# Optimization experiments

Hardware: AMD Instinct MI355X
Metric: run time of the kernel (lower is better)

## Reference

```python
import jax, jax.numpy as jnp
import numpy as np

NUM_CLUSTERS = 64
DIM = 512
ALPHA = 100.0
EPS = 1e-12  # torch F.normalize eps


def setup_inputs() -> dict:
    key = jax.random.key(0)
    k1, k2 = jax.random.split(key)
    x1 = jax.random.normal(k1, (30, DIM, 28, 28), dtype=jnp.float32)
    centroids = jax.random.uniform(k2, (NUM_CLUSTERS, DIM), dtype=jnp.float32)
    # _init_params: conv weight = 2*alpha*centroids (1x1 conv), bias = -alpha*||centroid||
    conv_w = 2.0 * ALPHA * centroids
    conv_b = -ALPHA * jnp.linalg.norm(centroids, axis=1)
    return {"x1": x1, "centroids": centroids, "conv_w": conv_w, "conv_b": conv_b}


def _l2norm(v, axis):
    n = jnp.sqrt(jnp.sum(v * v, axis=axis, keepdims=True))
    return v / jnp.maximum(n, EPS)


def reference(x1, centroids, conv_w, conv_b):
    T, C, H, W = x1.shape
    K, D = centroids.shape
    x = x1.reshape(T, C, H * W)            # [T, C, N]
    x = _l2norm(x, axis=1)                 # normalize_input: L2 over channel dim
    # 1x1 conv == matmul over channels: logits [T, K, N]
    logits = jnp.einsum('kc,tcn->tkn', conv_w, x) + conv_b[None, :, None]
    a = jax.nn.softmax(logits, axis=1)     # soft assignment over clusters
    # vlad[t,k,c] = sum_n a[t,k,n]*(x[t,c,n] - centroids[k,c])
    # rewritten as two small matmuls, avoiding the [K,C,N] residual tensor
    vlad = jnp.einsum('tkn,tcn->tkc', a, x) - a.sum(axis=-1)[:, :, None] * centroids[None]
    vlad = _l2norm(vlad, axis=2)           # intra-normalization over feature dim
    v = vlad.reshape(T, K * D)
    v = _l2norm(v, axis=1)                 # global L2 normalization
    return v.sum(axis=0, keepdims=True)    # [1, K*D] accumulated over 30 timesteps
```

## Files before the change

kernel.cpp:

```cpp
#include <hip/hip_runtime.h>
#include <math.h>

#define T_ 30
#define C_ 512
#define N_ 784
#define NA_ 800
#define XPITCH 520
#define EPSV 1e-12f

typedef __attribute__((ext_vector_type(8))) short bf16x8;
typedef __attribute__((ext_vector_type(4))) float f32x4;

__device__ __forceinline__ unsigned short f2bf(float f) {
    union { float f; unsigned int u; } v; v.f = f;
    unsigned int r = (v.u + 0x7FFFu + ((v.u >> 16) & 1u)) >> 16;
    return (unsigned short)r;
}
__device__ __forceinline__ float bf2f(unsigned short h) {
    union { unsigned int u; float f; } v; v.u = ((unsigned int)h) << 16;
    return v.f;
}

__global__ void k_prep(const float* __restrict__ w, unsigned short* __restrict__ wh,
                       unsigned short* __restrict__ wl) {
    int idx = blockIdx.x * 256 + threadIdx.x;
    float v = w[idx];
    unsigned short h = f2bf(v);
    wh[idx] = h;
    wl[idx] = f2bf(v - bf2f(h));
}

__global__ __launch_bounds__(256) void k_assign(
    const float* __restrict__ x, const unsigned short* __restrict__ wh,
    const unsigned short* __restrict__ wl, const float* __restrict__ b,
    unsigned short* __restrict__ aT, float* __restrict__ asum)
{
    __shared__ __align__(16) char smem[2 * 16 * XPITCH * 2];
    unsigned short* xh = (unsigned short*)smem;
    unsigned short* xl = xh + 16 * XPITCH;
    float* red = (float*)smem;
    __shared__ float ssq[4][16];
    __shared__ float invl[16];

    int t = blockIdx.y, n0 = blockIdx.x * 16;
    int tid = threadIdx.x;
    int w = tid >> 6, L = tid & 63, lid = L & 15, quad = L >> 4;

    int nseg = (tid & 3) * 4;
    int crow = tid >> 2;
    float ss0 = 0.f, ss1 = 0.f, ss2 = 0.f, ss3 = 0.f;
    #pragma unroll
    for (int p = 0; p < 8; ++p) {
        int c = p * 64 + crow;
        float4 q = *reinterpret_cast<const float4*>(
            x + ((size_t)t * C_ + c) * N_ + n0 + nseg);
        ss0 = fmaf(q.x, q.x, ss0); ss1 = fmaf(q.y, q.y, ss1);
        ss2 = fmaf(q.z, q.z, ss2); ss3 = fmaf(q.w, q.w, ss3);
        float vv[4] = {q.x, q.y, q.z, q.w};
        #pragma unroll
        for (int j = 0; j < 4; ++j) {
            unsigned short h = f2bf(vv[j]);
            xh[(nseg + j) * XPITCH + c] = h;
            xl[(nseg + j) * XPITCH + c] = f2bf(vv[j] - bf2f(h));
        }
    }
    #pragma unroll
    for (int m = 4; m <= 32; m <<= 1) {
        ss0 += __shfl_xor(ss0, m, 64); ss1 += __shfl_xor(ss1, m, 64);
        ss2 += __shfl_xor(ss2, m, 64); ss3 += __shfl_xor(ss3, m, 64);
    }
    if (L < 4) {
        ssq[w][L * 4 + 0] = ss0; ssq[w][L * 4 + 1] = ss1;
        ssq[w][L * 4 + 2] = ss2; ssq[w][L * 4 + 3] = ss3;
    }
    __syncthreads();
    if (tid < 16) {
        float s = ssq[0][tid] + ssq[1][tid] + ssq[2][tid] + ssq[3][tid];
        invl[tid] = 1.0f / fmaxf(sqrtf(s), EPSV);
    }

    f32x4 acc[4];
    #pragma unroll
    for (int mt = 0; mt < 4; ++mt)
        #pragma unroll
        for (int r = 0; r < 4; ++r) acc[mt][r] = 0.f;

    #pragma unroll
    for (int ks = 0; ks < 4; ++ks) {
        int cs = w * 128 + ks * 32;
        bf16x8 bh = *reinterpret_cast<const bf16x8*>(&xh[lid * XPITCH + cs + quad * 8]);
        bf16x8 bl = *reinterpret_cast<const bf16x8*>(&xl[lid * XPITCH + cs + quad * 8]);
        #pragma unroll
        for (int mt = 0; mt < 4; ++mt) {
            bf16x8 ah = *reinterpret_cast<const bf16x8*>(wh + (size_t)(mt * 16 + lid) * C_ + cs + quad * 8);
            bf16x8 al = *reinterpret_cast<const bf16x8*>(wl + (size_t)(mt * 16 + lid) * C_ + cs + quad * 8);
            acc[mt] = __builtin_amdgcn_mfma_f32_16x16x32_bf16(ah, bh, acc[mt], 0, 0, 0);
            acc[mt] = __builtin_amdgcn_mfma_f32_16x16x32_bf16(al, bh, acc[mt], 0, 0, 0);
            acc[mt] = __builtin_amdgcn_mfma_f32_16x16x32_bf16(ah, bl, acc[mt], 0, 0, 0);
        }
    }
    __syncthreads();
    {
        float* rp = red + w * (16 * 68);
        #pragma unroll
        for (int mt = 0; mt < 4; ++mt)
            *reinterpret_cast<f32x4*>(&rp[lid * 68 + mt * 16 + quad * 4]) = acc[mt];
    }
    __syncthreads();

    float bk = b[L];
    float asl = 0.f;
    unsigned short av[4];
    #pragma unroll
    for (int i = 0; i < 4; ++i) {
        int n = w * 4 + i;
        float v = red[0 * 1088 + n * 68 + L] + red[1 * 1088 + n * 68 + L]
                + red[2 * 1088 + n * 68 + L] + red[3 * 1088 + n * 68 + L];
        float inv = invl[n];
        v = fmaf(v, inv, bk);
        float mx = v;
        #pragma unroll
        for (int m = 1; m <= 32; m <<= 1) mx = fmaxf(mx, __shfl_xor(mx, m, 64));
        float e = __expf(v - mx);
        float se = e;
        #pragma unroll
        for (int m = 1; m <= 32; m <<= 1) se += __shfl_xor(se, m, 64);
        float a = e / se;
        av[i] = f2bf(a * inv);
        asl += a;
    }
    atomicAdd(&asum[t * 64 + L], asl);
    ushort4 st; st.x = av[0]; st.y = av[1]; st.z = av[2]; st.w = av[3];
    *reinterpret_cast<ushort4*>(aT + ((size_t)t * 64 + L) * NA_ + n0 + w * 4) = st;
}

__global__ __launch_bounds__(256) void k_vlad(
    const float* __restrict__ x, const unsigned short* __restrict__ aT,
    const float* __restrict__ asum, const float* __restrict__ cent,
    float* __restrict__ vlad, float* __restrict__ g2)
{
    __shared__ float red[4][16 * 68];
    int t = blockIdx.y, c0 = blockIdx.x * 16;
    int tid = threadIdx.x;
    int w = tid >> 6, L = tid & 63, lid = L & 15, quad = L >> 4;

    f32x4 acc[4];
    #pragma unroll
    for (int mt = 0; mt < 4; ++mt)
        #pragma unroll
        for (int r = 0; r < 4; ++r) acc[mt][r] = 0.f;

    const float* xrow = x + ((size_t)t * C_ + c0 + lid) * N_;
    const unsigned short* ab = aT + (size_t)t * 64 * NA_;

    for (int s = w; s < 25; s += 4) {
        int nb = s * 32 + quad * 8;
        int nbc = nb > 776 ? 776 : nb;
        float4 x0 = *reinterpret_cast<const float4*>(xrow + nbc);
        float4 x1 = *reinterpret_cast<const float4*>(xrow + nbc + 4);
        bf16x8 bb;
        bb[0] = (short)f2bf(x0.x); bb[1] = (short)f2bf(x0.y);
        bb[2] = (short)f2bf(x0.z); bb[3] = (short)f2bf(x0.w);
        bb[4] = (short)f2bf(x1.x); bb[5] = (short)f2bf(x1.y);
        bb[6] = (short)f2bf(x1.z); bb[7] = (short)f2bf(x1.w);
        #pragma unroll
        for (int mt = 0; mt < 4; ++mt) {
            bf16x8 af = *reinterpret_cast<const bf16x8*>(ab + (size_t)(mt * 16 + lid) * NA_ + nb);
            acc[mt] = __builtin_amdgcn_mfma_f32_16x16x32_bf16(af, bb, acc[mt], 0, 0, 0);
        }
    }
    {
        float* rp = &red[w][0];
        #pragma unroll
        for (int mt = 0; mt < 4; ++mt)
            *reinterpret_cast<f32x4*>(&rp[lid * 68 + mt * 16 + quad * 4]) = acc[mt];
    }
    __syncthreads();

    int k = tid >> 2, cs4 = (tid & 3) * 4;
    float as = asum[t * 64 + k];
    float4 cv = *reinterpret_cast<const float4*>(cent + k * C_ + c0 + cs4);
    float4 vout;
    float s2 = 0.f;
    #pragma unroll
    for (int j = 0; j < 4; ++j) {
        int cc = cs4 + j;
        float v = red[0][cc * 68 + k] + red[1][cc * 68 + k]
                + red[2][cc * 68 + k] + red[3][cc * 68 + k];
        v -= as * ((const float*)&cv)[j];
        ((float*)&vout)[j] = v;
        s2 = fmaf(v, v, s2);
    }
    *reinterpret_cast<float4*>(vlad + ((size_t)t * 64 + k) * C_ + c0 + cs4) = vout;
    s2 += __shfl_xor(s2, 1, 64);
    s2 += __shfl_xor(s2, 2, 64);
    if ((tid & 3) == 0) atomicAdd(&g2[t * 64 + k], s2);
}

__global__ __launch_bounds__(256) void k_out(
    const float* __restrict__ vlad, const float* __restrict__ g2,
    float* __restrict__ out)
{
    __shared__ float intr[1920];
    __shared__ float gl[1920];
    __shared__ float sinv[T_];
    int tid = threadIdx.x;
    for (int i = tid; i < 1920; i += 256) {
        float s = g2[i];
        gl[i] = s;
        intr[i] = 1.0f / fmaxf(sqrtf(s), EPSV);
    }
    __syncthreads();
    if (tid < T_) {
        float s = 0.f;
        #pragma unroll 8
        for (int k = 0; k < 64; ++k) {
            float iv = intr[tid * 64 + k];
            s += gl[tid * 64 + k] * iv * iv;
        }
        sinv[tid] = 1.0f / fmaxf(sqrtf(s), EPSV);
    }
    __syncthreads();
    int idx = blockIdx.x * 256 + tid;
    int k = idx >> 9;
    float s = 0.f;
    #pragma unroll 5
    for (int t = 0; t < T_; ++t)
        s += vlad[(size_t)t * 32768 + idx] * intr[t * 64 + k] * sinv[t];
    out[idx] = s;
}

extern "C" void kernel_launch(void* const* d_in, const int* in_sizes, int n_in,
                              void* d_out, int out_size, void* d_ws, size_t ws_size,
                              hipStream_t stream) {
    const float* x    = (const float*)d_in[0];
    const float* cent = (const float*)d_in[1];
    const float* w    = (const float*)d_in[2];
    const float* b    = (const float*)d_in[3];
    float* out = (float*)d_out;

    char* p = (char*)d_ws;
    unsigned short* wh = (unsigned short*)p;  p += 65536;
    unsigned short* wl = (unsigned short*)p;  p += 65536;
    float* asum = (float*)p;                  p += 1920 * 4;
    float* g2   = (float*)p;                  p += 1920 * 4;
    unsigned short* aT = (unsigned short*)p;  p += (size_t)T_ * 64 * NA_ * 2;
    float* vlad = (float*)p;                  p += (size_t)T_ * 64 * C_ * 4;

    k_prep<<<128, 256, 0, stream>>>(w, wh, wl);
    hipMemsetAsync(asum, 0, 2 * 1920 * 4, stream);
    hipMemsetAsync(aT, 0, (size_t)T_ * 64 * NA_ * 2, stream);
    k_assign<<<dim3(49, T_), 256, 0, stream>>>(x, wh, wl, b, aT, asum);
    k_vlad<<<dim3(32, T_), 256, 0, stream>>>(x, aT, asum, cent, vlad, g2);
    k_out<<<128, 256, 0, stream>>>(vlad, g2, out);
}
```

Before: 150.9 us.

## Add transpose pre-pass producing bf16 split layouts and column sum-of-squares

Adds a new kernel that reads x once, transposes it through shared memory into channel-contiguous bf16 hi/lo arrays for the assignment GEMM, writes a bf16 N-major copy for the VLAD GEMM, and accumulates per-pixel sum of squares with atomics. k_assign then loads operands straight from global memory instead of doing a strided fp32 gather and an in-LDS transpose. k_vlad reads pre-converted bf16 instead of converting fp32 on the fly. The cost is an extra launch plus writing and re-reading about three bf16 copies of x, which is more total memory traffic.

```diff
diff --git a/kernel.cpp b/kernel.cpp
--- a/kernel.cpp
+++ b/kernel.cpp
@@ -4,8 +4,8 @@
 #define T_ 30
 #define C_ 512
 #define N_ 784
+#define NP_ 832
 #define NA_ 800
-#define XPITCH 520
 #define EPSV 1e-12f
 
 typedef __attribute__((ext_vector_type(8))) short bf16x8;
@@ -30,54 +30,86 @@
     wl[idx] = f2bf(v - bf2f(h));
 }
 
+__global__ __launch_bounds__(256) void k_trans(
+    const float* __restrict__ x, unsigned short* __restrict__ xh,
+    unsigned short* __restrict__ xl, unsigned short* __restrict__ xbn,
+    float* __restrict__ sumsq)
+{
+    __shared__ float sx[64][65];
+    __shared__ float wred[4][64];
+    int n0 = blockIdx.x * 64, c0 = blockIdx.y * 64, t = blockIdx.z;
+    int tid = threadIdx.x;
+    int cr = tid >> 4, li = tid & 15;
+    int w = tid >> 6;
+    float ss[4] = {0.f, 0.f, 0.f, 0.f};
+
+    #pragma unroll
+    for (int j = 0; j < 4; ++j) {
+        int cl = j * 16 + cr;
+        int n = n0 + li * 4;
+        float4 q = make_float4(0.f, 0.f, 0.f, 0.f);
+        if (n < N_)
+            q = *reinterpret_cast<const float4*>(x + ((size_t)t * C_ + c0 + cl) * N_ + n);
+        ss[0] = fmaf(q.x, q.x, ss[0]); ss[1] = fmaf(q.y, q.y, ss[1]);
+        ss[2] = fmaf(q.z, q.z, ss[2]); ss[3] = fmaf(q.w, q.w, ss[3]);
+        sx[cl][li * 4 + 0] = q.x; sx[cl][li * 4 + 1] = q.y;
+        sx[cl][li * 4 + 2] = q.z; sx[cl][li * 4 + 3] = q.w;
+    }
+    #pragma unroll
+    for (int i = 0; i < 4; ++i) {
+        ss[i] += __shfl_xor(ss[i], 16, 64);
+        ss[i] += __shfl_xor(ss[i], 32, 64);
+    }
+    if (((tid >> 4) & 3) == 0) {
+        wred[w][li * 4 + 0] = ss[0]; wred[w][li * 4 + 1] = ss[1];
+        wred[w][li * 4 + 2] = ss[2]; wred[w][li * 4 + 3] = ss[3];
+    }
+    __syncthreads();
+    if (tid < 64 && n0 + tid < N_) {
+        float s = wred[0][tid] + wred[1][tid] + wred[2][tid] + wred[3][tid];
+        atomicAdd(&sumsq[t * N_ + n0 + tid], s);
+    }
+    {
+        int li2 = tid & 15, nr = tid >> 4;
+        #pragma unroll
+        for (int j = 0; j < 4; ++j) {
+            int nl = nr + j * 16;
+            float v0 = sx[li2 * 4 + 0][nl], v1 = sx[li2 * 4 + 1][nl];
+            float v2 = sx[li2 * 4 + 2][nl], v3 = sx[li2 * 4 + 3][nl];
+            ushort4 h, l;
+            h.x = f2bf(v0); l.x = f2bf(v0 - bf2f(h.x));
+            h.y = f2bf(v1); l.y = f2bf(v1 - bf2f(h.y));
+            h.z = f2bf(v2); l.z = f2bf(v2 - bf2f(h.z));
+            h.w = f2bf(v3); l.w = f2bf(v3 - bf2f(h.w));
+            size_t o = ((size_t)t * NP_ + n0 + nl) * C_ + c0 + li2 * 4;
+            *reinterpret_cast<ushort4*>(xh + o) = h;
+            *reinterpret_cast<ushort4*>(xl + o) = l;
+        }
+    }
+    #pragma unroll
+    for (int j = 0; j < 4; ++j) {
+        int cl = j * 16 + cr;
+        int n = n0 + li * 4;
+        if (n < NA_) {
+            ushort4 h;
+            h.x = f2bf(sx[cl][li * 4 + 0]); h.y = f2bf(sx[cl][li * 4 + 1]);
+            h.z = f2bf(sx[cl][li * 4 + 2]); h.w = f2bf(sx[cl][li * 4 + 3]);
+            *reinterpret_cast<ushort4*>(xbn + ((size_t)t * C_ + c0 + cl) * NA_ + n) = h;
+        }
+    }
+}
+
 __global__ __launch_bounds__(256) void k_assign(
-    const float* __restrict__ x, const unsigned short* __restrict__ wh,
-    const unsigned short* __restrict__ wl, const float* __restrict__ b,
+    const unsigned short* __restrict__ xh, const unsigned short* __restrict__ xl,
+    const unsigned short* __restrict__ wh, const unsigned short* __restrict__ wl,
+    const float* __restrict__ b, const float* __restrict__ sumsq,
     unsigned short* __restrict__ aT, float* __restrict__ asum)
 {
-    __shared__ __align__(16) char smem[2 * 16 * XPITCH * 2];
-    unsigned short* xh = (unsigned short*)smem;
-    unsigned short* xl = xh + 16 * XPITCH;
-    float* red = (float*)smem;
-    __shared__ float ssq[4][16];
-    __shared__ float invl[16];
-
+    __shared__ float red[4 * 16 * 68];
     int t = blockIdx.y, n0 = blockIdx.x * 16;
     int tid = threadIdx.x;
     int w = tid >> 6, L = tid & 63, lid = L & 15, quad = L >> 4;
-
-    int nseg = (tid & 3) * 4;
-    int crow = tid >> 2;
-    float ss0 = 0.f, ss1 = 0.f, ss2 = 0.f, ss3 = 0.f;
-    #pragma unroll
-    for (int p = 0; p < 8; ++p) {
-        int c = p * 64 + crow;
-        float4 q = *reinterpret_cast<const float4*>(
-            x + ((size_t)t * C_ + c) * N_ + n0 + nseg);
-        ss0 = fmaf(q.x, q.x, ss0); ss1 = fmaf(q.y, q.y, ss1);
-        ss2 = fmaf(q.z, q.z, ss2); ss3 = fmaf(q.w, q.w, ss3);
-        float vv[4] = {q.x, q.y, q.z, q.w};
-        #pragma unroll
-        for (int j = 0; j < 4; ++j) {
-            unsigned short h = f2bf(vv[j]);
-            xh[(nseg + j) * XPITCH + c] = h;
-            xl[(nseg + j) * XPITCH + c] = f2bf(vv[j] - bf2f(h));
-        }
-    }
-    #pragma unroll
-    for (int m = 4; m <= 32; m <<= 1) {
-        ss0 += __shfl_xor(ss0, m, 64); ss1 += __shfl_xor(ss1, m, 64);
-        ss2 += __shfl_xor(ss2, m, 64); ss3 += __shfl_xor(ss3, m, 64);
-    }
-    if (L < 4) {
-        ssq[w][L * 4 + 0] = ss0; ssq[w][L * 4 + 1] = ss1;
-        ssq[w][L * 4 + 2] = ss2; ssq[w][L * 4 + 3] = ss3;
-    }
-    __syncthreads();
-    if (tid < 16) {
-        float s = ssq[0][tid] + ssq[1][tid] + ssq[2][tid] + ssq[3][tid];
-        invl[tid] = 1.0f / fmaxf(sqrtf(s), EPSV);
-    }
+    int n_lane = n0 + lid;
 
     f32x4 acc[4];
     #pragma unroll
@@ -85,23 +117,25 @@
         #pragma unroll
         for (int r = 0; r < 4; ++r) acc[mt][r] = 0.f;
 
+    const unsigned short* bp  = xh + ((size_t)t * NP_ + n_lane) * C_ + w * 128 + quad * 8;
+    const unsigned short* blp = xl + ((size_t)t * NP_ + n_lane) * C_ + w * 128 + quad * 8;
+
     #pragma unroll
     for (int ks = 0; ks < 4; ++ks) {
-        int cs = w * 128 + ks * 32;
-        bf16x8 bh = *reinterpret_cast<const bf16x8*>(&xh[lid * XPITCH + cs + quad * 8]);
-        bf16x8 bl = *reinterpret_cast<const bf16x8*>(&xl[lid * XPITCH + cs + quad * 8]);
+        bf16x8 bh = *reinterpret_cast<const bf16x8*>(bp + ks * 32);
+        bf16x8 bl = *reinterpret_cast<const bf16x8*>(blp + ks * 32);
+        int cs = w * 128 + ks * 32 + quad * 8;
         #pragma unroll
         for (int mt = 0; mt < 4; ++mt) {
-            bf16x8 ah = *reinterpret_cast<const bf16x8*>(wh + (size_t)(mt * 16 + lid) * C_ + cs + quad * 8);
-            bf16x8 al = *reinterpret_cast<const bf16x8*>(wl + (size_t)(mt * 16 + lid) * C_ + cs + quad * 8);
+            bf16x8 ah = *reinterpret_cast<const bf16x8*>(wh + (size_t)(mt * 16 + lid) * C_ + cs);
+            bf16x8 al = *reinterpret_cast<const bf16x8*>(wl + (size_t)(mt * 16 + lid) * C_ + cs);
             acc[mt] = __builtin_amdgcn_mfma_f32_16x16x32_bf16(ah, bh, acc[mt], 0, 0, 0);
             acc[mt] = __builtin_amdgcn_mfma_f32_16x16x32_bf16(al, bh, acc[mt], 0, 0, 0);
             acc[mt] = __builtin_amdgcn_mfma_f32_16x16x32_bf16(ah, bl, acc[mt], 0, 0, 0);
         }
     }
-    __syncthreads();
     {
-        float* rp = red + w * (16 * 68);
+        float* rp = red + w * 1088;
         #pragma unroll
         for (int mt = 0; mt < 4; ++mt)
             *reinterpret_cast<f32x4*>(&rp[lid * 68 + mt * 16 + quad * 4]) = acc[mt];
@@ -116,7 +150,8 @@
         int n = w * 4 + i;
         float v = red[0 * 1088 + n * 68 + L] + red[1 * 1088 + n * 68 + L]
                 + red[2 * 1088 + n * 68 + L] + red[3 * 1088 + n * 68 + L];
-        float inv = invl[n];
+        float s = sumsq[t * N_ + n0 + n];
+        float inv = 1.0f / fmaxf(sqrtf(s), EPSV);
         v = fmaf(v, inv, bk);
         float mx = v;
         #pragma unroll
@@ -135,7 +170,7 @@
 }
 
 __global__ __launch_bounds__(256) void k_vlad(
-    const float* __restrict__ x, const unsigned short* __restrict__ aT,
+    const unsigned short* __restrict__ xbn, const unsigned short* __restrict__ aT,
     const float* __restrict__ asum, const float* __restrict__ cent,
     float* __restrict__ vlad, float* __restrict__ g2)
 {
@@ -150,19 +185,13 @@
         #pragma unroll
         for (int r = 0; r < 4; ++r) acc[mt][r] = 0.f;
 
-    const float* xrow = x + ((size_t)t * C_ + c0 + lid) * N_;
-    const unsigned short* ab = aT + (size_t)t * 64 * NA_;
-
+    const unsigned short* xr = xbn + ((size_t)t * C_ + c0 + lid) * NA_ + quad * 8;
+    const unsigned short* ab = aT + (size_t)t * 64 * NA_ + quad * 8;
+
+    #pragma unroll 2
     for (int s = w; s < 25; s += 4) {
-        int nb = s * 32 + quad * 8;
-        int nbc = nb > 776 ? 776 : nb;
-        float4 x0 = *reinterpret_cast<const float4*>(xrow + nbc);
-        float4 x1 = *reinterpret_cast<const float4*>(xrow + nbc + 4);
-        bf16x8 bb;
-        bb[0] = (short)f2bf(x0.x); bb[1] = (short)f2bf(x0.y);
-        bb[2] = (short)f2bf(x0.z); bb[3] = (short)f2bf(x0.w);
-        bb[4] = (short)f2bf(x1.x); bb[5] = (short)f2bf(x1.y);
-        bb[6] = (short)f2bf(x1.z); bb[7] = (short)f2bf(x1.w);
+        int nb = s * 32;
+        bf16x8 bb = *reinterpret_cast<const bf16x8*>(xr + nb);
         #pragma unroll
         for (int mt = 0; mt < 4; ++mt) {
             bf16x8 af = *reinterpret_cast<const bf16x8*>(ab + (size_t)(mt * 16 + lid) * NA_ + nb);
@@ -242,15 +271,20 @@
     char* p = (char*)d_ws;
     unsigned short* wh = (unsigned short*)p;  p += 65536;
     unsigned short* wl = (unsigned short*)p;  p += 65536;
-    float* asum = (float*)p;                  p += 1920 * 4;
-    float* g2   = (float*)p;                  p += 1920 * 4;
-    unsigned short* aT = (unsigned short*)p;  p += (size_t)T_ * 64 * NA_ * 2;
+    float* sumsq = (float*)p;                 p += 30 * 784 * 4;
+    float* asum  = (float*)p;                 p += 1920 * 4;
+    float* g2    = (float*)p;                 p += 1920 * 4;
+    unsigned short* aT  = (unsigned short*)p; p += (size_t)T_ * 64 * NA_ * 2;
+    unsigned short* xh  = (unsigned short*)p; p += (size_t)T_ * NP_ * C_ * 2;
+    unsigned short* xl  = (unsigned short*)p; p += (size_t)T_ * NP_ * C_ * 2;
+    unsigned short* xbn = (unsigned short*)p; p += (size_t)T_ * C_ * NA_ * 2;
     float* vlad = (float*)p;                  p += (size_t)T_ * 64 * C_ * 4;
 
     k_prep<<<128, 256, 0, stream>>>(w, wh, wl);
-    hipMemsetAsync(asum, 0, 2 * 1920 * 4, stream);
+    hipMemsetAsync(sumsq, 0, (30 * 784 + 2 * 1920) * 4, stream);
     hipMemsetAsync(aT, 0, (size_t)T_ * 64 * NA_ * 2, stream);
-    k_assign<<<dim3(49, T_), 256, 0, stream>>>(x, wh, wl, b, aT, asum);
-    k_vlad<<<dim3(32, T_), 256, 0, stream>>>(x, aT, asum, cent, vlad, g2);
+    k_trans<<<dim3(13, 8, T_), 256, 0, stream>>>(x, xh, xl, xbn, sumsq);
+    k_assign<<<dim3(49, T_), 256, 0, stream>>>(xh, xl, wh, wl, b, sumsq, aT, asum);
+    k_vlad<<<dim3(32, T_), 256, 0, stream>>>(xbn, aT, asum, cent, vlad, g2);
     k_out<<<128, 256, 0, stream>>>(vlad, g2, out);
 }
```

After: 163.1 us. +8.1%, slower.

## Retile assignment kernel to 64 positions per block with per-wave full reduction

Applied to the files above, without the earlier changes.

k_assign now handles 64 spatial positions per block instead of 16. Each wave owns 16 positions and accumulates the full channel reduction over four staged LDS chunks. The hi/lo bf16 split of x is packed into one 32-bit LDS word, and softmax runs directly from the MFMA accumulators. This removes the cross-wave LDS reduction and cuts redundant weight reloads per block. Padded positions are written as zeros, so the separate aT memset is dropped, and k_out loses one shared array. The cost is fewer blocks (390), which lowers parallelism, plus narrower scattered aT stores.

```diff
diff --git a/kernel.cpp b/kernel.cpp
--- a/kernel.cpp
+++ b/kernel.cpp
@@ -4,12 +4,13 @@
 #define T_ 30
 #define C_ 512
 #define N_ 784
-#define NA_ 800
-#define XPITCH 520
+#define NA_ 832
+#define PITCH 129
 #define EPSV 1e-12f
 
 typedef __attribute__((ext_vector_type(8))) short bf16x8;
 typedef __attribute__((ext_vector_type(4))) float f32x4;
+typedef __attribute__((ext_vector_type(4))) int i32x4;
 
 __device__ __forceinline__ unsigned short f2bf(float f) {
     union { float f; unsigned int u; } v; v.f = f;
@@ -35,49 +36,16 @@
     const unsigned short* __restrict__ wl, const float* __restrict__ b,
     unsigned short* __restrict__ aT, float* __restrict__ asum)
 {
-    __shared__ __align__(16) char smem[2 * 16 * XPITCH * 2];
-    unsigned short* xh = (unsigned short*)smem;
-    unsigned short* xl = xh + 16 * XPITCH;
-    float* red = (float*)smem;
-    __shared__ float ssq[4][16];
-    __shared__ float invl[16];
-
-    int t = blockIdx.y, n0 = blockIdx.x * 16;
+    __shared__ unsigned int xpk[64 * PITCH];
+    __shared__ float ssq[64];
+    int t = blockIdx.y, n0 = blockIdx.x * 64;
     int tid = threadIdx.x;
     int w = tid >> 6, L = tid & 63, lid = L & 15, quad = L >> 4;
-
-    int nseg = (tid & 3) * 4;
-    int crow = tid >> 2;
-    float ss0 = 0.f, ss1 = 0.f, ss2 = 0.f, ss3 = 0.f;
-    #pragma unroll
-    for (int p = 0; p < 8; ++p) {
-        int c = p * 64 + crow;
-        float4 q = *reinterpret_cast<const float4*>(
-            x + ((size_t)t * C_ + c) * N_ + n0 + nseg);
-        ss0 = fmaf(q.x, q.x, ss0); ss1 = fmaf(q.y, q.y, ss1);
-        ss2 = fmaf(q.z, q.z, ss2); ss3 = fmaf(q.w, q.w, ss3);
-        float vv[4] = {q.x, q.y, q.z, q.w};
-        #pragma unroll
-        for (int j = 0; j < 4; ++j) {
-            unsigned short h = f2bf(vv[j]);
-            xh[(nseg + j) * XPITCH + c] = h;
-            xl[(nseg + j) * XPITCH + c] = f2bf(vv[j] - bf2f(h));
-        }
-    }
-    #pragma unroll
-    for (int m = 4; m <= 32; m <<= 1) {
-        ss0 += __shfl_xor(ss0, m, 64); ss1 += __shfl_xor(ss1, m, 64);
-        ss2 += __shfl_xor(ss2, m, 64); ss3 += __shfl_xor(ss3, m, 64);
-    }
-    if (L < 4) {
-        ssq[w][L * 4 + 0] = ss0; ssq[w][L * 4 + 1] = ss1;
-        ssq[w][L * 4 + 2] = ss2; ssq[w][L * 4 + 3] = ss3;
-    }
-    __syncthreads();
-    if (tid < 16) {
-        float s = ssq[0][tid] + ssq[1][tid] + ssq[2][tid] + ssq[3][tid];
-        invl[tid] = 1.0f / fmaxf(sqrtf(s), EPSV);
-    }
+    int nseg = (tid & 15) * 4;
+    int crow = tid >> 4;
+
+    if (tid < 64) ssq[tid] = 0.f;
+    float ss[4] = {0.f, 0.f, 0.f, 0.f};
 
     f32x4 acc[4];
     #pragma unroll
@@ -85,53 +53,104 @@
         #pragma unroll
         for (int r = 0; r < 4; ++r) acc[mt][r] = 0.f;
 
-    #pragma unroll
-    for (int ks = 0; ks < 4; ++ks) {
-        int cs = w * 128 + ks * 32;
-        bf16x8 bh = *reinterpret_cast<const bf16x8*>(&xh[lid * XPITCH + cs + quad * 8]);
-        bf16x8 bl = *reinterpret_cast<const bf16x8*>(&xl[lid * XPITCH + cs + quad * 8]);
-        #pragma unroll
-        for (int mt = 0; mt < 4; ++mt) {
-            bf16x8 ah = *reinterpret_cast<const bf16x8*>(wh + (size_t)(mt * 16 + lid) * C_ + cs + quad * 8);
-            bf16x8 al = *reinterpret_cast<const bf16x8*>(wl + (size_t)(mt * 16 + lid) * C_ + cs + quad * 8);
-            acc[mt] = __builtin_amdgcn_mfma_f32_16x16x32_bf16(ah, bh, acc[mt], 0, 0, 0);
-            acc[mt] = __builtin_amdgcn_mfma_f32_16x16x32_bf16(al, bh, acc[mt], 0, 0, 0);
-            acc[mt] = __builtin_amdgcn_mfma_f32_16x16x32_bf16(ah, bl, acc[mt], 0, 0, 0);
-        }
-    }
-    __syncthreads();
-    {
-        float* rp = red + w * (16 * 68);
-        #pragma unroll
-        for (int mt = 0; mt < 4; ++mt)
-            *reinterpret_cast<f32x4*>(&rp[lid * 68 + mt * 16 + quad * 4]) = acc[mt];
-    }
-    __syncthreads();
-
-    float bk = b[L];
-    float asl = 0.f;
-    unsigned short av[4];
-    #pragma unroll
-    for (int i = 0; i < 4; ++i) {
-        int n = w * 4 + i;
-        float v = red[0 * 1088 + n * 68 + L] + red[1 * 1088 + n * 68 + L]
-                + red[2 * 1088 + n * 68 + L] + red[3 * 1088 + n * 68 + L];
-        float inv = invl[n];
-        v = fmaf(v, inv, bk);
-        float mx = v;
-        #pragma unroll
-        for (int m = 1; m <= 32; m <<= 1) mx = fmaxf(mx, __shfl_xor(mx, m, 64));
-        float e = __expf(v - mx);
-        float se = e;
-        #pragma unroll
-        for (int m = 1; m <= 32; m <<= 1) se += __shfl_xor(se, m, 64);
-        float a = e / se;
-        av[i] = f2bf(a * inv);
-        asl += a;
-    }
-    atomicAdd(&asum[t * 64 + L], asl);
-    ushort4 st; st.x = av[0]; st.y = av[1]; st.z = av[2]; st.w = av[3];
-    *reinterpret_cast<ushort4*>(aT + ((size_t)t * 64 + L) * NA_ + n0 + w * 4) = st;
+    for (int cc = 0; cc < 4; ++cc) {
+        #pragma unroll
+        for (int p = 0; p < 8; ++p) {
+            int cl = p * 16 + crow;
+            int c = cc * 128 + cl;
+            int n = n0 + nseg;
+            float4 q = make_float4(0.f, 0.f, 0.f, 0.f);
+            if (n < N_)
+                q = *reinterpret_cast<const float4*>(x + ((size_t)t * C_ + c) * N_ + n);
+            float vv[4] = {q.x, q.y, q.z, q.w};
+            #pragma unroll
+            for (int j = 0; j < 4; ++j) {
+                float v = vv[j];
+                ss[j] = fmaf(v, v, ss[j]);
+                union { float f; unsigned int u; } cv; cv.f = v;
+                unsigned int hiw = cv.u & 0xFFFF0000u;
+                union { unsigned int u; float f; } hv; hv.u = hiw;
+                unsigned int lo = f2bf(v - hv.f);
+                xpk[(nseg + j) * PITCH + cl] = hiw | lo;
+            }
+        }
+        if (cc == 3) {
+            #pragma unroll
+            for (int j = 0; j < 4; ++j) {
+                ss[j] += __shfl_xor(ss[j], 16, 64);
+                ss[j] += __shfl_xor(ss[j], 32, 64);
+            }
+            if ((tid & 48) == 0) {
+                #pragma unroll
+                for (int j = 0; j < 4; ++j) atomicAdd(&ssq[nseg + j], ss[j]);
+            }
+        }
+        __syncthreads();
+        #pragma unroll
+        for (int ks = 0; ks < 4; ++ks) {
+            int cl0 = ks * 32 + quad * 8;
+            unsigned int u[8];
+            #pragma unroll
+            for (int e = 0; e < 8; ++e)
+                u[e] = xpk[(w * 16 + lid) * PITCH + cl0 + e];
+            union { i32x4 v; bf16x8 b; } bh, bl;
+            #pragma unroll
+            for (int e2 = 0; e2 < 4; ++e2) {
+                bh.v[e2] = (int)((u[2 * e2] >> 16) | (u[2 * e2 + 1] & 0xFFFF0000u));
+                bl.v[e2] = (int)((u[2 * e2] & 0xFFFFu) | (u[2 * e2 + 1] << 16));
+            }
+            int cs = cc * 128 + ks * 32 + quad * 8;
+            #pragma unroll
+            for (int mt = 0; mt < 4; ++mt) {
+                bf16x8 ah = *reinterpret_cast<const bf16x8*>(wh + (size_t)(mt * 16 + lid) * C_ + cs);
+                bf16x8 al = *reinterpret_cast<const bf16x8*>(wl + (size_t)(mt * 16 + lid) * C_ + cs);
+                acc[mt] = __builtin_amdgcn_mfma_f32_16x16x32_bf16(ah, bh.b, acc[mt], 0, 0, 0);
+                acc[mt] = __builtin_amdgcn_mfma_f32_16x16x32_bf16(al, bh.b, acc[mt], 0, 0, 0);
+                acc[mt] = __builtin_amdgcn_mfma_f32_16x16x32_bf16(ah, bl.b, acc[mt], 0, 0, 0);
+            }
+        }
+        __syncthreads();
+    }
+
+    int n_lane = n0 + w * 16 + lid;
+    bool valid = n_lane < N_;
+    float inv = 0.f;
+    if (valid) inv = 1.0f / fmaxf(sqrtf(ssq[w * 16 + lid]), EPSV);
+
+    float lg[16];
+    float mx = -1e30f;
+    #pragma unroll
+    for (int mt = 0; mt < 4; ++mt) {
+        f32x4 bv = *reinterpret_cast<const f32x4*>(b + mt * 16 + quad * 4);
+        #pragma unroll
+        for (int r = 0; r < 4; ++r) {
+            float v = fmaf(acc[mt][r], inv, bv[r]);
+            lg[mt * 4 + r] = v;
+            mx = fmaxf(mx, v);
+        }
+    }
+    mx = fmaxf(mx, __shfl_xor(mx, 16, 64));
+    mx = fmaxf(mx, __shfl_xor(mx, 32, 64));
+    float se = 0.f;
+    #pragma unroll
+    for (int u = 0; u < 16; ++u) { lg[u] = __expf(lg[u] - mx); se += lg[u]; }
+    se += __shfl_xor(se, 16, 64);
+    se += __shfl_xor(se, 32, 64);
+    float rs = 1.0f / se;
+
+    size_t abase = (size_t)t * 64 * NA_ + n_lane;
+    #pragma unroll
+    for (int mt = 0; mt < 4; ++mt)
+        #pragma unroll
+        for (int r = 0; r < 4; ++r) {
+            int k = mt * 16 + quad * 4 + r;
+            float a = lg[mt * 4 + r] * rs;
+            aT[abase + (size_t)k * NA_] = valid ? f2bf(a * inv) : (unsigned short)0;
+            float ak = valid ? a : 0.f;
+            ak += __shfl_xor(ak, 1, 64); ak += __shfl_xor(ak, 2, 64);
+            ak += __shfl_xor(ak, 4, 64); ak += __shfl_xor(ak, 8, 64);
+            if (lid == 0) atomicAdd(&asum[t * 64 + k], ak);
+        }
 }
 
 __global__ __launch_bounds__(256) void k_vlad(
@@ -153,7 +172,7 @@
     const float* xrow = x + ((size_t)t * C_ + c0 + lid) * N_;
     const unsigned short* ab = aT + (size_t)t * 64 * NA_;
 
-    for (int s = w; s < 25; s += 4) {
+    for (int s = w; s < 26; s += 4) {
         int nb = s * 32 + quad * 8;
         int nbc = nb > 776 ? 776 : nb;
         float4 x0 = *reinterpret_cast<const float4*>(xrow + nbc);
@@ -202,21 +221,17 @@
     float* __restrict__ out)
 {
     __shared__ float intr[1920];
-    __shared__ float gl[1920];
     __shared__ float sinv[T_];
     int tid = threadIdx.x;
-    for (int i = tid; i < 1920; i += 256) {
-        float s = g2[i];
-        gl[i] = s;
-        intr[i] = 1.0f / fmaxf(sqrtf(s), EPSV);
-    }
+    for (int i = tid; i < 1920; i += 256)
+        intr[i] = 1.0f / fmaxf(sqrtf(g2[i]), EPSV);
     __syncthreads();
     if (tid < T_) {
         float s = 0.f;
         #pragma unroll 8
         for (int k = 0; k < 64; ++k) {
             float iv = intr[tid * 64 + k];
-            s += gl[tid * 64 + k] * iv * iv;
+            s += g2[tid * 64 + k] * iv * iv;
         }
         sinv[tid] = 1.0f / fmaxf(sqrtf(s), EPSV);
     }
@@ -249,8 +264,7 @@
 
     k_prep<<<128, 256, 0, stream>>>(w, wh, wl);
     hipMemsetAsync(asum, 0, 2 * 1920 * 4, stream);
-    hipMemsetAsync(aT, 0, (size_t)T_ * 64 * NA_ * 2, stream);
-    k_assign<<<dim3(49, T_), 256, 0, stream>>>(x, wh, wl, b, aT, asum);
+    k_assign<<<dim3(13, T_), 256, 0, stream>>>(x, wh, wl, b, aT, asum);
     k_vlad<<<dim3(32, T_), 256, 0, stream>>>(x, aT, asum, cent, vlad, g2);
     k_out<<<128, 256, 0, stream>>>(vlad, g2, out);
 }
```

After: 155.2 us. 1.03x slower.
